# Kernel tuning notes

Measured on AMD Instinct MI355X. Metric: run time of the kernel, lower is better.

The kernel has to match this reference:

```python
import jax, jax.numpy as jnp
import numpy as np

M = 16                      # multiplicity of each irrep block
INV3 = 1.0 / np.sqrt(3.0)   # w3j(1,1,0) component-normalized
INV2 = 1.0 / np.sqrt(2.0)   # w3j(1,1,1) component-normalized
A0 = 1.0 / np.sqrt(2.0 * M) # fan-in norm for 0e outputs (2 paths x mul 16)
A1 = 1.0 / np.sqrt(3.0 * M) # fan-in norm for 1o outputs (3 paths x mul 16)


def setup_inputs() -> dict:
    E, N, ED, HID = 100000, 10000, 32, 128
    WNUM = 2 * M * (2 * M) + 3 * M * M  # 1792 per-edge TP weights
    ks = jax.random.split(jax.random.key(0), 10)
    return {
        "dst": jax.random.randint(ks[0], (E,), 0, N),
        "x_src": jax.random.normal(ks[1], (E, 4 * M), jnp.float32),   # 16x0e+16x1o
        "x_dst": jax.random.normal(ks[2], (N, 4 * M), jnp.float32),
        "sh": jax.random.normal(ks[3], (E, 4), jnp.float32),          # 1x0e+1x1o
        "edge_attr": jax.random.normal(ks[4], (E, ED), jnp.float32),
        "We1": jax.random.normal(ks[5], (ED, HID), jnp.float32) / np.sqrt(ED),
        "be1": jnp.zeros((HID,), jnp.float32),
        "We2": jax.random.normal(ks[6], (HID, WNUM), jnp.float32) / np.sqrt(HID),
        "be2": jnp.zeros((WNUM,), jnp.float32),
        "Wr0": jax.random.normal(ks[7], (M, 2 * M), jnp.float32),     # 16x0e -> 32x0e
        "Wr1": jax.random.normal(ks[8], (M, M), jnp.float32),         # 16x1o -> 16x1o
    }


def _forward(dst, x_src, x_dst, sh, edge_attr, We1, be1, We2, be2, Wr0, Wr1):
    E = x_src.shape[0]
    N = x_dst.shape[0]
    o0 = 2 * M  # 32x0e tp output (scalars + gates)

    # edge MLP -> per-edge tensor-product weights [E, 1792]
    w = jax.nn.relu(edge_attr @ We1 + be1) @ We2 + be2
    i = 0
    w_ss = w[:, i:i + M * o0].reshape(E, M, o0); i += M * o0   # 0e x 0e -> 0e
    w_vv0 = w[:, i:i + M * o0].reshape(E, M, o0); i += M * o0  # 1o x 1o -> 0e
    w_sv = w[:, i:i + M * M].reshape(E, M, M); i += M * M      # 0e x 1o -> 1o
    w_vs = w[:, i:i + M * M].reshape(E, M, M); i += M * M      # 1o x 0e -> 1o
    w_vv1 = w[:, i:i + M * M].reshape(E, M, M)                 # 1o x 1o -> 1o

    s1 = x_src[:, :M]                       # [E, 16]
    v1 = x_src[:, M:].reshape(E, M, 3)      # [E, 16, 3]
    s2 = sh[:, 0]                           # [E]
    v2 = sh[:, 1:4]                         # [E, 3]

    # fully-connected tensor product with per-edge weights
    out0 = A0 * (jnp.einsum('em,emo->eo', s1 * s2[:, None], w_ss)
                 + INV3 * jnp.einsum('emc,ec,emo->eo', v1, v2, w_vv0))  # [E, 32]
    cross = jnp.cross(v1, v2[:, None, :])   # [E, 16, 3]
    out1 = A1 * (jnp.einsum('em,ec,emo->eoc', s1, v2, w_sv)
                 + jnp.einsum('emc,e,emo->eoc', v1, s2, w_vs)
                 + INV2 * jnp.einsum('emc,emo->eoc', cross, w_vv1))     # [E, 16, 3]
    msg = jnp.concatenate([out0, out1.reshape(E, -1)], axis=1)          # [E, 80]

    # scatter-mean over destination nodes
    ssum = jax.ops.segment_sum(msg, dst, num_segments=N)
    cnt = jax.ops.segment_sum(jnp.ones((E,), msg.dtype), dst, num_segments=N)
    msg = ssum / jnp.maximum(cnt, 1.0)[:, None]                          # [N, 80]

    # residual equivariant linear on x_dst
    sd = x_dst[:, :M]
    vd = x_dst[:, M:].reshape(N, M, 3)
    res0 = (sd @ Wr0) / np.sqrt(M)                                       # [N, 32]
    res1 = jnp.einsum('nmc,mo->noc', vd, Wr1) / np.sqrt(M)               # [N, 16, 3]
    msg = msg + jnp.concatenate([res0, res1.reshape(N, -1)], axis=1)

    # gate nonlinearity: relu(scalars), sigmoid(gates) * gated vectors
    scalars = jax.nn.relu(msg[:, :M])
    gates = jax.nn.sigmoid(msg[:, M:2 * M])
    gated = msg[:, 2 * M:].reshape(N, M, 3) * gates[:, :, None]
    return jnp.concatenate([scalars, gated.reshape(N, -1)], axis=1)      # [N, 64]


def reference(dst, x_src, x_dst, sh, edge_attr, We1, be1, We2, be2, Wr0, Wr1):
    return _forward(dst, x_src, x_dst, sh, edge_attr, We1, be1, We2, be2, Wr0, Wr1)
```

## Files before the change

### kernel.cpp

```cpp
#include <hip/hip_runtime.h>
#include <math.h>

#define WNUM 1792
#define HID 128

#define INV3C 0.5773502691896258f
#define INV2C 0.7071067811865476f
#define A0C   0.17677669529663687f
#define A1C   0.14433756729740643f
#define MAXDEG 64

typedef short bf8 __attribute__((ext_vector_type(8)));
typedef _Float16 f16x8 __attribute__((ext_vector_type(8)));
typedef _Float16 f16x4 __attribute__((ext_vector_type(4)));
typedef float f32x4 __attribute__((ext_vector_type(4)));

__device__ inline unsigned short f2bf(float f) {
  union { float f; unsigned u; } v; v.f = f;
  unsigned r = v.u + 0x7FFFu + ((v.u >> 16) & 1u);
  return (unsigned short)(r >> 16);
}
__device__ inline float bf2f(unsigned short h) {
  union { unsigned u; float f; } v; v.u = ((unsigned)h) << 16;
  return v.f;
}
__device__ inline float wscale(int t) {
  if (t < 32) return A0C;
  if (t < 64) return A0C * INV3C;
  if (t < 96) return A1C;
  return A1C * INV2C;
}

__global__ __launch_bounds__(256) void prep_kernel(
    const float* __restrict__ We1, const float* __restrict__ We2,
    const float* __restrict__ be2,
    unsigned short* __restrict__ we1x, _Float16* __restrict__ we2h,
    float* __restrict__ be2p, int* __restrict__ cntp, int N)
{
  int i = blockIdx.x * 256 + threadIdx.x;
  if (i < 28672) {
    int t = i >> 8, c = (i >> 6) & 3, lane = i & 63;
    int quad = lane >> 4, l15 = lane & 15;
    int col = t * 16 + l15;
    float sc = wscale(t);
    f16x8 v;
    #pragma unroll
    for (int j = 0; j < 8; ++j) {
      int k = c * 32 + quad * 8 + j;
      v[j] = (_Float16)(We2[(size_t)k * WNUM + col] * sc);
    }
    *(f16x8*)(we2h + (size_t)t * 2048 + c * 512 + lane * 8) = v;
  } else if (i < 29184) {
    int q = i - 28672;
    int c1 = q >> 6, lane = q & 63;
    int quad = lane >> 4, l15 = lane & 15;
    int col = c1 * 16 + l15;
    bf8 hh, ll;
    #pragma unroll
    for (int j = 0; j < 8; ++j) {
      int k = quad * 8 + j;
      float v = We1[k * HID + col];
      unsigned short hi = f2bf(v);
      hh[j] = (short)hi;
      ll[j] = (short)f2bf(v - bf2f(hi));
    }
    *(bf8*)(we1x + c1 * 1024 + lane * 8) = hh;
    *(bf8*)(we1x + c1 * 1024 + 512 + lane * 8) = ll;
  } else if (i < 30976) {
    int q = i - 29184;
    int t = q >> 4, l16 = q & 15;
    be2p[(t >> 1) * 32 + l16 * 2 + (t & 1)] = be2[q] * wscale(t);
  } else if (i < 30976 + N) {
    cntp[i - 30976] = 0;
  }
}

__device__ inline void chains2(const f16x8* a0, const f16x8* a1,
    f16x8 b0, f16x8 b1, f16x8 b2, f16x8 b3,
    f16x8 b4, f16x8 b5, f16x8 b6, f16x8 b7,
    float2 bias, f32x4* wa, f32x4* wb)
{
  f32x4 ca0 = {bias.x, bias.x, bias.x, bias.x};
  f32x4 cb0 = {bias.y, bias.y, bias.y, bias.y};
  f32x4 ca1 = ca0, cb1 = cb0;
  ca0 = __builtin_amdgcn_mfma_f32_16x16x32_f16(a0[0], b0, ca0, 0, 0, 0);
  cb0 = __builtin_amdgcn_mfma_f32_16x16x32_f16(a0[0], b4, cb0, 0, 0, 0);
  ca1 = __builtin_amdgcn_mfma_f32_16x16x32_f16(a1[0], b0, ca1, 0, 0, 0);
  cb1 = __builtin_amdgcn_mfma_f32_16x16x32_f16(a1[0], b4, cb1, 0, 0, 0);
  ca0 = __builtin_amdgcn_mfma_f32_16x16x32_f16(a0[1], b1, ca0, 0, 0, 0);
  cb0 = __builtin_amdgcn_mfma_f32_16x16x32_f16(a0[1], b5, cb0, 0, 0, 0);
  ca1 = __builtin_amdgcn_mfma_f32_16x16x32_f16(a1[1], b1, ca1, 0, 0, 0);
  cb1 = __builtin_amdgcn_mfma_f32_16x16x32_f16(a1[1], b5, cb1, 0, 0, 0);
  ca0 = __builtin_amdgcn_mfma_f32_16x16x32_f16(a0[2], b2, ca0, 0, 0, 0);
  cb0 = __builtin_amdgcn_mfma_f32_16x16x32_f16(a0[2], b6, cb0, 0, 0, 0);
  ca1 = __builtin_amdgcn_mfma_f32_16x16x32_f16(a1[2], b2, ca1, 0, 0, 0);
  cb1 = __builtin_amdgcn_mfma_f32_16x16x32_f16(a1[2], b6, cb1, 0, 0, 0);
  ca0 = __builtin_amdgcn_mfma_f32_16x16x32_f16(a0[3], b3, ca0, 0, 0, 0);
  cb0 = __builtin_amdgcn_mfma_f32_16x16x32_f16(a0[3], b7, cb0, 0, 0, 0);
  ca1 = __builtin_amdgcn_mfma_f32_16x16x32_f16(a1[3], b3, ca1, 0, 0, 0);
  cb1 = __builtin_amdgcn_mfma_f32_16x16x32_f16(a1[3], b7, cb1, 0, 0, 0);
  wa[0] = ca0; wb[0] = cb0; wa[1] = ca1; wb[1] = cb1;
}

__device__ inline void pair_mm(const _Float16* bL, const float* bp, int p,
                               const f16x8 (&af)[2][4], f32x4* wa, f32x4* wb)
{
  f16x8 b0 = *(const f16x8*)(bL);
  f16x8 b1 = *(const f16x8*)(bL + 512);
  f16x8 b2 = *(const f16x8*)(bL + 1024);
  f16x8 b3 = *(const f16x8*)(bL + 1536);
  f16x8 b4 = *(const f16x8*)(bL + 2048);
  f16x8 b5 = *(const f16x8*)(bL + 2560);
  f16x8 b6 = *(const f16x8*)(bL + 3072);
  f16x8 b7 = *(const f16x8*)(bL + 3584);
  float2 bias2 = *(const float2*)(bp + p * 32);
  chains2(af[0], af[1], b0, b1, b2, b3, b4, b5, b6, b7, bias2, wa, wb);
}

template <bool MSG>
__global__ __launch_bounds__(256, 2) void edge_kernel(
    const float* __restrict__ ea, const float* __restrict__ xsrc,
    const float* __restrict__ sh, const int* __restrict__ dst,
    const float* __restrict__ be1,
    const unsigned short* __restrict__ we1x, const _Float16* __restrict__ we2h,
    const float* __restrict__ be2p,
    float* __restrict__ outp, int* __restrict__ eidx, int* __restrict__ cntp, int E)
{
  const int lane = threadIdx.x & 63;
  const int w    = threadIdx.x >> 6;
  const int quad = lane >> 4;
  const int l16  = lane & 15;
  const int eb   = (blockIdx.x * 4 + w) * 32;

  __shared__ union SMem {
    _Float16 h[4][32][136];
    _Float16 B[4][4096];
  } uS;
  __shared__ _Float16 fss_s[4][16][32];
  __shared__ _Float16 fvv_s[4][16][32];
  __shared__ _Float16 s1h_s[4][16][32];
  __shared__ _Float16 v1h_s[4][16][3][32];
  __shared__ float4 vq_s[4][32];

  #define STAGE_PAIR(p) { \
    const _Float16* gsrc_ = we2h + (size_t)(p) * 4096; \
    _Float16* ldst_ = &uS.B[(p) & 3][0]; \
    __builtin_amdgcn_global_load_lds( \
      (const __attribute__((address_space(1))) void*)(gsrc_ + (w * 2) * 512 + lane * 8), \
      (__attribute__((address_space(3))) void*)(ldst_ + (w * 2) * 512), 16, 0, 0); \
    __builtin_amdgcn_global_load_lds( \
      (const __attribute__((address_space(1))) void*)(gsrc_ + (w * 2 + 1) * 512 + lane * 8), \
      (__attribute__((address_space(3))) void*)(ldst_ + (w * 2 + 1) * 512), 16, 0, 0); \
  }

  if (lane < 32) {
    int ge = eb + lane;
    if (ge < E) {
      int node = dst[ge];
      int pos = atomicAdd(cntp + node, 1);
      if (MSG) { if (pos < MAXDEG) eidx[node * MAXDEG + pos] = ge; }
    }
  }

  {
    int e2 = lane >> 1, mg = lane & 1;
    int ge = eb + e2;
    if (ge < E) {
      const float* xp = xsrc + (size_t)ge * 64;
      float4 sq0 = *(const float4*)(xp + mg * 8);
      float4 sq1 = *(const float4*)(xp + mg * 8 + 4);
      float s1a[8] = {sq0.x,sq0.y,sq0.z,sq0.w,sq1.x,sq1.y,sq1.z,sq1.w};
      const float* vp = xp + 16 + mg * 24;
      float la[24];
      #pragma unroll
      for (int qv = 0; qv < 6; ++qv) {
        float4 t = *(const float4*)(vp + qv * 4);
        la[qv*4+0] = t.x; la[qv*4+1] = t.y; la[qv*4+2] = t.z; la[qv*4+3] = t.w;
      }
      float4 shq = *(const float4*)(sh + (size_t)ge * 4);
      float s2 = shq.x, v2x = shq.y, v2y = shq.z, v2z = shq.w;
      #pragma unroll
      for (int mi = 0; mi < 8; ++mi) {
        int m = mg * 8 + mi;
        float v1x = la[mi*3], v1y = la[mi*3+1], v1z = la[mi*3+2];
        fss_s[w][m][e2] = (_Float16)(s1a[mi] * s2);
        fvv_s[w][m][e2] = (_Float16)(v1x*v2x + v1y*v2y + v1z*v2z);
        s1h_s[w][m][e2] = (_Float16)s1a[mi];
        v1h_s[w][m][0][e2] = (_Float16)v1x;
        v1h_s[w][m][1][e2] = (_Float16)v1y;
        v1h_s[w][m][2][e2] = (_Float16)v1z;
      }
      if (mg == 0) vq_s[w][e2] = make_float4(v2x, v2y, v2z, s2);
    } else {
      #pragma unroll
      for (int mi = 0; mi < 8; ++mi) {
        int m = mg * 8 + mi;
        fss_s[w][m][e2] = (_Float16)0.f;
        fvv_s[w][m][e2] = (_Float16)0.f;
        s1h_s[w][m][e2] = (_Float16)0.f;
        v1h_s[w][m][0][e2] = (_Float16)0.f;
        v1h_s[w][m][1][e2] = (_Float16)0.f;
        v1h_s[w][m][2][e2] = (_Float16)0.f;
      }
      if (mg == 0) vq_s[w][e2] = make_float4(0,0,0,0);
    }
  }

  {
    bf8 ah[2], al[2];
    #pragma unroll
    for (int g = 0; g < 2; ++g) {
      int gea = eb + g * 16 + l16; if (gea > E - 1) gea = E - 1;
      const float* ep = ea + (size_t)gea * 32 + quad * 8;
      float4 p0 = *(const float4*)ep;
      float4 p1 = *(const float4*)(ep + 4);
      float pv[8] = {p0.x,p0.y,p0.z,p0.w,p1.x,p1.y,p1.z,p1.w};
      #pragma unroll
      for (int j = 0; j < 8; ++j) {
        unsigned short hi = f2bf(pv[j]);
        ah[g][j] = (short)hi;
        al[g][j] = (short)f2bf(pv[j] - bf2f(hi));
      }
    }
    const unsigned short* wb1 = we1x + lane * 8;
    #pragma unroll 2
    for (int c = 0; c < 8; ++c) {
      bf8 bh = *(const bf8*)(wb1 + c * 1024);
      bf8 bl = *(const bf8*)(wb1 + c * 1024 + 512);
      float bias = be1[c * 16 + l16];
      #pragma unroll
      for (int g = 0; g < 2; ++g) {
        f32x4 hc = {bias, bias, bias, bias};
        hc = __builtin_amdgcn_mfma_f32_16x16x32_bf16(al[g], bh, hc, 0, 0, 0);
        hc = __builtin_amdgcn_mfma_f32_16x16x32_bf16(ah[g], bl, hc, 0, 0, 0);
        hc = __builtin_amdgcn_mfma_f32_16x16x32_bf16(ah[g], bh, hc, 0, 0, 0);
        #pragma unroll
        for (int r = 0; r < 4; ++r)
          uS.h[w][g * 16 + quad * 4 + r][c * 16 + l16] = (_Float16)fmaxf(hc[r], 0.f);
      }
    }
  }
  __syncthreads();

  f16x8 af[2][4];
  #pragma unroll
  for (int g = 0; g < 2; ++g)
    #pragma unroll
    for (int ch = 0; ch < 4; ++ch)
      af[g][ch] = *(const f16x8*)&uS.h[w][g * 16 + l16][ch * 32 + quad * 8];
  __syncthreads();

  STAGE_PAIR(0)
  STAGE_PAIR(1)
  __syncthreads();

  const float* bp = be2p + l16 * 2;
  float m0a[2][4] = {{0,0,0,0},{0,0,0,0}}, m0b[2][4] = {{0,0,0,0},{0,0,0,0}};

  #pragma unroll 1
  for (int i = 0; i < 16; i += 2) {
    STAGE_PAIR(i + 2)
    STAGE_PAIR(i + 3)
    f32x4 wa[2], wb[2];
    pair_mm(&uS.B[i & 3][lane * 8], bp, i, af, wa, wb);
    #pragma unroll
    for (int g = 0; g < 2; ++g) {
      f16x4 fv = *(const f16x4*)&fss_s[w][i][g * 16 + quad * 4];
      #pragma unroll
      for (int r = 0; r < 4; ++r) {
        float f = (float)fv[r];
        m0a[g][r] = fmaf(wa[g][r], f, m0a[g][r]);
        m0b[g][r] = fmaf(wb[g][r], f, m0b[g][r]);
      }
    }
    pair_mm(&uS.B[(i + 1) & 3][lane * 8], bp, i + 1, af, wa, wb);
    #pragma unroll
    for (int g = 0; g < 2; ++g) {
      f16x4 fv = *(const f16x4*)&fss_s[w][i + 1][g * 16 + quad * 4];
      #pragma unroll
      for (int r = 0; r < 4; ++r) {
        float f = (float)fv[r];
        m0a[g][r] = fmaf(wa[g][r], f, m0a[g][r]);
        m0b[g][r] = fmaf(wb[g][r], f, m0b[g][r]);
      }
    }
    __syncthreads();
  }

  #pragma unroll 1
  for (int i = 0; i < 16; i += 2) {
    int pg = 16 + i;
    STAGE_PAIR(pg + 2)
    STAGE_PAIR(pg + 3)
    f32x4 wa[2], wb[2];
    pair_mm(&uS.B[pg & 3][lane * 8], bp, pg, af, wa, wb);
    #pragma unroll
    for (int g = 0; g < 2; ++g) {
      f16x4 fv = *(const f16x4*)&fvv_s[w][i][g * 16 + quad * 4];
      #pragma unroll
      for (int r = 0; r < 4; ++r) {
        float f = (float)fv[r];
        m0a[g][r] = fmaf(wa[g][r], f, m0a[g][r]);
        m0b[g][r] = fmaf(wb[g][r], f, m0b[g][r]);
      }
    }
    pair_mm(&uS.B[(pg + 1) & 3][lane * 8], bp, pg + 1, af, wa, wb);
    #pragma unroll
    for (int g = 0; g < 2; ++g) {
      f16x4 fv = *(const f16x4*)&fvv_s[w][i + 1][g * 16 + quad * 4];
      #pragma unroll
      for (int r = 0; r < 4; ++r) {
        float f = (float)fv[r];
        m0a[g][r] = fmaf(wa[g][r], f, m0a[g][r]);
        m0b[g][r] = fmaf(wb[g][r], f, m0b[g][r]);
      }
    }
    __syncthreads();
  }

  #pragma unroll
  for (int g = 0; g < 2; ++g)
    #pragma unroll
    for (int r = 0; r < 4; ++r) {
      int ge = eb + g * 16 + quad * 4 + r;
      if (ge < E) {
        if (MSG) {
          float* mp = outp + (size_t)ge * 80;
          mp[l16]      = m0a[g][r];
          mp[16 + l16] = m0b[g][r];
        } else {
          float* ap = outp + (size_t)dst[ge] * 80;
          atomicAdd(ap + l16,      m0a[g][r]);
          atomicAdd(ap + 16 + l16, m0b[g][r]);
        }
      }
    }

  float sg[2][4] = {{0,0,0,0},{0,0,0,0}};
  #pragma unroll 1
  for (int i = 0; i < 8; i += 2) {
    int pg = 32 + i;
    STAGE_PAIR(pg + 2)
    STAGE_PAIR(pg + 3)
    f32x4 wa[2], wb[2];
    pair_mm(&uS.B[pg & 3][lane * 8], bp, pg, af, wa, wb);
    #pragma unroll
    for (int g = 0; g < 2; ++g) {
      f16x4 sA = *(const f16x4*)&s1h_s[w][2*i][g * 16 + quad * 4];
      f16x4 sB = *(const f16x4*)&s1h_s[w][2*i + 1][g * 16 + quad * 4];
      #pragma unroll
      for (int r = 0; r < 4; ++r)
        sg[g][r] = fmaf(wb[g][r], (float)sB[r], fmaf(wa[g][r], (float)sA[r], sg[g][r]));
    }
    pair_mm(&uS.B[(pg + 1) & 3][lane * 8], bp, pg + 1, af, wa, wb);
    #pragma unroll
    for (int g = 0; g < 2; ++g) {
      f16x4 sA = *(const f16x4*)&s1h_s[w][2*i + 2][g * 16 + quad * 4];
      f16x4 sB = *(const f16x4*)&s1h_s[w][2*i + 3][g * 16 + quad * 4];
      #pragma unroll
      for (int r = 0; r < 4; ++r)
        sg[g][r] = fmaf(wb[g][r], (float)sB[r], fmaf(wa[g][r], (float)sA[r], sg[g][r]));
    }
    __syncthreads();
  }
  float4 vq[2][4];
  #pragma unroll
  for (int g = 0; g < 2; ++g)
    #pragma unroll
    for (int r = 0; r < 4; ++r) vq[g][r] = vq_s[w][g * 16 + quad * 4 + r];

  float m1x[2][4], m1y[2][4], m1z[2][4];
  #pragma unroll
  for (int g = 0; g < 2; ++g)
    #pragma unroll
    for (int r = 0; r < 4; ++r) {
      m1x[g][r] = sg[g][r] * vq[g][r].x;
      m1y[g][r] = sg[g][r] * vq[g][r].y;
      m1z[g][r] = sg[g][r] * vq[g][r].z;
    }

  #pragma unroll
  for (int sec = 0; sec < 2; ++sec) {
    float ux[2][4] = {{0,0,0,0},{0,0,0,0}}, uy[2][4] = {{0,0,0,0},{0,0,0,0}},
          uz[2][4] = {{0,0,0,0},{0,0,0,0}};
    int base = 40 + sec * 8;
    #pragma unroll 1
    for (int i = 0; i < 8; i += 2) {
      int pg = base + i;
      if (pg + 2 < 56) STAGE_PAIR(pg + 2)
      if (pg + 3 < 56) STAGE_PAIR(pg + 3)
      f32x4 wa[2], wb[2];
      pair_mm(&uS.B[pg & 3][lane * 8], bp, pg, af, wa, wb);
      #pragma unroll
      for (int g = 0; g < 2; ++g) {
        f16x4 xA = *(const f16x4*)&v1h_s[w][2*i][0][g*16 + quad*4];
        f16x4 xB = *(const f16x4*)&v1h_s[w][2*i+1][0][g*16 + quad*4];
        f16x4 yA = *(const f16x4*)&v1h_s[w][2*i][1][g*16 + quad*4];
        f16x4 yB = *(const f16x4*)&v1h_s[w][2*i+1][1][g*16 + quad*4];
        f16x4 zA = *(const f16x4*)&v1h_s[w][2*i][2][g*16 + quad*4];
        f16x4 zB = *(const f16x4*)&v1h_s[w][2*i+1][2][g*16 + quad*4];
        #pragma unroll
        for (int r = 0; r < 4; ++r) {
          ux[g][r] = fmaf(wb[g][r], (float)xB[r], fmaf(wa[g][r], (float)xA[r], ux[g][r]));
          uy[g][r] = fmaf(wb[g][r], (float)yB[r], fmaf(wa[g][r], (float)yA[r], uy[g][r]));
          uz[g][r] = fmaf(wb[g][r], (float)zB[r], fmaf(wa[g][r], (float)zA[r], uz[g][r]));
        }
      }
      pair_mm(&uS.B[(pg + 1) & 3][lane * 8], bp, pg + 1, af, wa, wb);
      #pragma unroll
      for (int g = 0; g < 2; ++g) {
        f16x4 xA = *(const f16x4*)&v1h_s[w][2*i+2][0][g*16 + quad*4];
        f16x4 xB = *(const f16x4*)&v1h_s[w][2*i+3][0][g*16 + quad*4];
        f16x4 yA = *(const f16x4*)&v1h_s[w][2*i+2][1][g*16 + quad*4];
        f16x4 yB = *(const f16x4*)&v1h_s[w][2*i+3][1][g*16 + quad*4];
        f16x4 zA = *(const f16x4*)&v1h_s[w][2*i+2][2][g*16 + quad*4];
        f16x4 zB = *(const f16x4*)&v1h_s[w][2*i+3][2][g*16 + quad*4];
        #pragma unroll
        for (int r = 0; r < 4; ++r) {
          ux[g][r] = fmaf(wb[g][r], (float)xB[r], fmaf(wa[g][r], (float)xA[r], ux[g][r]));
          uy[g][r] = fmaf(wb[g][r], (float)yB[r], fmaf(wa[g][r], (float)yA[r], uy[g][r]));
          uz[g][r] = fmaf(wb[g][r], (float)zB[r], fmaf(wa[g][r], (float)zA[r], uz[g][r]));
        }
      }
      __syncthreads();
    }
    if (sec == 0) {
      #pragma unroll
      for (int g = 0; g < 2; ++g)
        #pragma unroll
        for (int r = 0; r < 4; ++r) {
          m1x[g][r] = fmaf(vq[g][r].w, ux[g][r], m1x[g][r]);
          m1y[g][r] = fmaf(vq[g][r].w, uy[g][r], m1y[g][r]);
          m1z[g][r] = fmaf(vq[g][r].w, uz[g][r], m1z[g][r]);
        }
    } else {
      #pragma unroll
      for (int g = 0; g < 2; ++g)
        #pragma unroll
        for (int r = 0; r < 4; ++r) {
          m1x[g][r] = fmaf(uy[g][r], vq[g][r].z, m1x[g][r]);
          m1x[g][r] = fmaf(-uz[g][r], vq[g][r].y, m1x[g][r]);
          m1y[g][r] = fmaf(uz[g][r], vq[g][r].x, m1y[g][r]);
          m1y[g][r] = fmaf(-ux[g][r], vq[g][r].z, m1y[g][r]);
          m1z[g][r] = fmaf(ux[g][r], vq[g][r].y, m1z[g][r]);
          m1z[g][r] = fmaf(-uy[g][r], vq[g][r].x, m1z[g][r]);
        }
    }
  }

  #pragma unroll
  for (int g = 0; g < 2; ++g)
    #pragma unroll
    for (int r = 0; r < 4; ++r) {
      int ge = eb + g * 16 + quad * 4 + r;
      if (ge < E) {
        if (MSG) {
          float* mp = outp + (size_t)ge * 80;
          mp[32 + l16*3 + 0] = m1x[g][r];
          mp[32 + l16*3 + 1] = m1y[g][r];
          mp[32 + l16*3 + 2] = m1z[g][r];
        } else {
          float* ap = outp + (size_t)dst[ge] * 80;
          atomicAdd(ap + 32 + l16*3 + 0, m1x[g][r]);
          atomicAdd(ap + 32 + l16*3 + 1, m1y[g][r]);
          atomicAdd(ap + 32 + l16*3 + 2, m1z[g][r]);
        }
      }
    }
  #undef STAGE_PAIR
}

__global__ __launch_bounds__(128) void node_gather_kernel(
    const float* __restrict__ msg, const int* __restrict__ eidx,
    const int* __restrict__ cntp,
    const float* __restrict__ xdst, const float* __restrict__ Wr0,
    const float* __restrict__ Wr1, float* __restrict__ out, int N)
{
  int n = blockIdx.x;
  if (n >= N) return;
  int j = threadIdx.x;
  int c0 = cntp[n];
  int deg = c0 < MAXDEG ? c0 : MAXDEG;
  float inv = 1.0f / fmaxf((float)c0, 1.0f);
  __shared__ float s_sum[80];
  if (j < 80) {
    float s = 0.f;
    const int* ep = eidx + (size_t)n * MAXDEG;
    int i = 0;
    for (; i + 1 < deg; i += 2) {
      int e0 = ep[i], e1 = ep[i + 1];
      s += msg[(size_t)e0 * 80 + j] + msg[(size_t)e1 * 80 + j];
    }
    if (i < deg) s += msg[(size_t)ep[i] * 80 + j];
    s_sum[j] = s * inv;
  }
  __syncthreads();
  if (j >= 64) return;
  const float* xd = xdst + (size_t)n * 64;
  float* op = out + (size_t)n * 64;
  if (j < 16) {
    float s = 0.f;
    #pragma unroll
    for (int m = 0; m < 16; ++m) s = fmaf(xd[m], Wr0[m * 32 + j], s);
    op[j] = fmaxf(s_sum[j] + 0.25f * s, 0.f);
  } else {
    int jj = j - 16;
    int o = (jj * 86) >> 8;
    int c = jj - o * 3;
    float tg = 0.f, v = 0.f;
    #pragma unroll
    for (int m = 0; m < 16; ++m) {
      tg = fmaf(xd[m], Wr0[m * 32 + 16 + o], tg);
      v  = fmaf(xd[16 + m * 3 + c], Wr1[m * 16 + o], v);
    }
    float g = 1.0f / (1.0f + expf(-(s_sum[16 + o] + 0.25f * tg)));
    op[16 + jj] = (s_sum[32 + jj] + 0.25f * v) * g;
  }
}

__global__ __launch_bounds__(256) void node_kernel(
    const float* __restrict__ accn, const int* __restrict__ cntp,
    const float* __restrict__ xdst, const float* __restrict__ Wr0,
    const float* __restrict__ Wr1, float* __restrict__ out, int N)
{
  int idx = blockIdx.x * 256 + threadIdx.x;
  int n = idx >> 6, j = idx & 63;
  if (n >= N) return;
  float inv = 1.0f / fmaxf((float)cntp[n], 1.0f);
  const float* ap = accn + (size_t)n * 80;
  const float* xd = xdst + (size_t)n * 64;
  float* op = out + (size_t)n * 64;
  if (j < 16) {
    float s = 0.f;
    #pragma unroll
    for (int m = 0; m < 16; ++m) s = fmaf(xd[m], Wr0[m * 32 + j], s);
    op[j] = fmaxf(ap[j] * inv + 0.25f * s, 0.f);
  } else {
    int jj = j - 16;
    int o = (jj * 86) >> 8;
    int c = jj - o * 3;
    float tg = 0.f, v = 0.f;
    #pragma unroll
    for (int m = 0; m < 16; ++m) {
      tg = fmaf(xd[m], Wr0[m * 32 + 16 + o], tg);
      v  = fmaf(xd[16 + m * 3 + c], Wr1[m * 16 + o], v);
    }
    float g = 1.0f / (1.0f + expf(-(ap[16 + o] * inv + 0.25f * tg)));
    op[16 + jj] = (ap[32 + jj] * inv + 0.25f * v) * g;
  }
}

extern "C" void kernel_launch(void* const* d_in, const int* in_sizes, int n_in,
                              void* d_out, int out_size, void* d_ws, size_t ws_size,
                              hipStream_t stream)
{
  const int*   dst  = (const int*)d_in[0];
  const float* xsrc = (const float*)d_in[1];
  const float* xdst = (const float*)d_in[2];
  const float* sh   = (const float*)d_in[3];
  const float* ea   = (const float*)d_in[4];
  const float* We1  = (const float*)d_in[5];
  const float* be1  = (const float*)d_in[6];
  const float* We2  = (const float*)d_in[7];
  const float* be2  = (const float*)d_in[8];
  const float* Wr0  = (const float*)d_in[9];
  const float* Wr1  = (const float*)d_in[10];
  const int E = in_sizes[0];
  const int N = in_sizes[2] / 64;

  char* ws = (char*)d_ws;
  _Float16* we2h = (_Float16*)ws;
  unsigned short* we1x = (unsigned short*)(ws + 458752);
  float* be2p = (float*)(ws + 475136);
  int*   cntp = (int*)(ws + 482560);
  size_t off = 482560 + (size_t)N * 4;
  off = (off + 15) & ~(size_t)15;

  size_t need_msg = off + (size_t)N * MAXDEG * 4 + (size_t)E * 80 * 4;
  bool use_msg = (ws_size >= need_msg);

  prep_kernel<<<(30976 + N + 255) / 256, 256, 0, stream>>>(We1, We2, be2,
      we1x, we2h, be2p, cntp, N);

  if (use_msg) {
    int* eidx = (int*)(ws + off);
    float* msg = (float*)(ws + off + (size_t)N * MAXDEG * 4);
    edge_kernel<true><<<(E + 127) / 128, 256, 0, stream>>>(ea, xsrc, sh, dst, be1,
        we1x, we2h, be2p, msg, eidx, cntp, E);
    node_gather_kernel<<<N, 128, 0, stream>>>(msg, eidx, cntp, xdst, Wr0, Wr1,
        (float*)d_out, N);
  } else {
    float* accn = (float*)(ws + off);
    hipMemsetAsync(accn, 0, (size_t)N * 320, stream);
    edge_kernel<false><<<(E + 127) / 128, 256, 0, stream>>>(ea, xsrc, sh, dst, be1,
        we1x, we2h, be2p, accn, (int*)nullptr, cntp, E);
    node_kernel<<<((size_t)N * 64 + 255) / 256, 256, 0, stream>>>(accn, cntp,
        xdst, Wr0, Wr1, (float*)d_out, N);
  }
}
```

Before: 199.5 us.

## Merge weight-generation phases into one loop with deeper staging and partial waitcnt barriers

Replaces the four separate loops over weight pairs (two steps per iteration, full __syncthreads) with a single 56-step loop. The loop stages pairs three ahead into the 4-slot ring buffer and syncs with explicit s_waitcnt on vmcnt plus s_barrier, so the newest global loads can stay in flight across the barrier. The aim is to keep more weight-staging loads outstanding and cut barrier drain stalls. In exchange the loop body carries branches on the phase index and holds all accumulators live at once, which raises register pressure, and the hand-coded waitcnt immediates must match the real number of loads issued per stage.

```diff
diff --git a/kernel.cpp b/kernel.cpp
--- a/kernel.cpp
+++ b/kernel.cpp
@@ -248,157 +248,76 @@
     #pragma unroll
     for (int ch = 0; ch < 4; ++ch)
       af[g][ch] = *(const f16x8*)&uS.h[w][g * 16 + l16][ch * 32 + quad * 8];
-  __syncthreads();
-
-  STAGE_PAIR(0)
-  STAGE_PAIR(1)
-  __syncthreads();
-
-  const float* bp = be2p + l16 * 2;
-  float m0a[2][4] = {{0,0,0,0},{0,0,0,0}}, m0b[2][4] = {{0,0,0,0},{0,0,0,0}};
-
-  #pragma unroll 1
-  for (int i = 0; i < 16; i += 2) {
-    STAGE_PAIR(i + 2)
-    STAGE_PAIR(i + 3)
-    f32x4 wa[2], wb[2];
-    pair_mm(&uS.B[i & 3][lane * 8], bp, i, af, wa, wb);
-    #pragma unroll
-    for (int g = 0; g < 2; ++g) {
-      f16x4 fv = *(const f16x4*)&fss_s[w][i][g * 16 + quad * 4];
-      #pragma unroll
-      for (int r = 0; r < 4; ++r) {
-        float f = (float)fv[r];
-        m0a[g][r] = fmaf(wa[g][r], f, m0a[g][r]);
-        m0b[g][r] = fmaf(wb[g][r], f, m0b[g][r]);
-      }
-    }
-    pair_mm(&uS.B[(i + 1) & 3][lane * 8], bp, i + 1, af, wa, wb);
-    #pragma unroll
-    for (int g = 0; g < 2; ++g) {
-      f16x4 fv = *(const f16x4*)&fss_s[w][i + 1][g * 16 + quad * 4];
-      #pragma unroll
-      for (int r = 0; r < 4; ++r) {
-        float f = (float)fv[r];
-        m0a[g][r] = fmaf(wa[g][r], f, m0a[g][r]);
-        m0b[g][r] = fmaf(wb[g][r], f, m0b[g][r]);
-      }
-    }
-    __syncthreads();
-  }
-
-  #pragma unroll 1
-  for (int i = 0; i < 16; i += 2) {
-    int pg = 16 + i;
-    STAGE_PAIR(pg + 2)
-    STAGE_PAIR(pg + 3)
-    f32x4 wa[2], wb[2];
-    pair_mm(&uS.B[pg & 3][lane * 8], bp, pg, af, wa, wb);
-    #pragma unroll
-    for (int g = 0; g < 2; ++g) {
-      f16x4 fv = *(const f16x4*)&fvv_s[w][i][g * 16 + quad * 4];
-      #pragma unroll
-      for (int r = 0; r < 4; ++r) {
-        float f = (float)fv[r];
-        m0a[g][r] = fmaf(wa[g][r], f, m0a[g][r]);
-        m0b[g][r] = fmaf(wb[g][r], f, m0b[g][r]);
-      }
-    }
-    pair_mm(&uS.B[(pg + 1) & 3][lane * 8], bp, pg + 1, af, wa, wb);
-    #pragma unroll
-    for (int g = 0; g < 2; ++g) {
-      f16x4 fv = *(const f16x4*)&fvv_s[w][i + 1][g * 16 + quad * 4];
-      #pragma unroll
-      for (int r = 0; r < 4; ++r) {
-        float f = (float)fv[r];
-        m0a[g][r] = fmaf(wa[g][r], f, m0a[g][r]);
-        m0b[g][r] = fmaf(wb[g][r], f, m0b[g][r]);
-      }
-    }
-    __syncthreads();
-  }
-
-  #pragma unroll
-  for (int g = 0; g < 2; ++g)
-    #pragma unroll
-    for (int r = 0; r < 4; ++r) {
-      int ge = eb + g * 16 + quad * 4 + r;
-      if (ge < E) {
-        if (MSG) {
-          float* mp = outp + (size_t)ge * 80;
-          mp[l16]      = m0a[g][r];
-          mp[16 + l16] = m0b[g][r];
-        } else {
-          float* ap = outp + (size_t)dst[ge] * 80;
-          atomicAdd(ap + l16,      m0a[g][r]);
-          atomicAdd(ap + 16 + l16, m0b[g][r]);
-        }
-      }
-    }
-
-  float sg[2][4] = {{0,0,0,0},{0,0,0,0}};
-  #pragma unroll 1
-  for (int i = 0; i < 8; i += 2) {
-    int pg = 32 + i;
-    STAGE_PAIR(pg + 2)
-    STAGE_PAIR(pg + 3)
-    f32x4 wa[2], wb[2];
-    pair_mm(&uS.B[pg & 3][lane * 8], bp, pg, af, wa, wb);
-    #pragma unroll
-    for (int g = 0; g < 2; ++g) {
-      f16x4 sA = *(const f16x4*)&s1h_s[w][2*i][g * 16 + quad * 4];
-      f16x4 sB = *(const f16x4*)&s1h_s[w][2*i + 1][g * 16 + quad * 4];
-      #pragma unroll
-      for (int r = 0; r < 4; ++r)
-        sg[g][r] = fmaf(wb[g][r], (float)sB[r], fmaf(wa[g][r], (float)sA[r], sg[g][r]));
-    }
-    pair_mm(&uS.B[(pg + 1) & 3][lane * 8], bp, pg + 1, af, wa, wb);
-    #pragma unroll
-    for (int g = 0; g < 2; ++g) {
-      f16x4 sA = *(const f16x4*)&s1h_s[w][2*i + 2][g * 16 + quad * 4];
-      f16x4 sB = *(const f16x4*)&s1h_s[w][2*i + 3][g * 16 + quad * 4];
-      #pragma unroll
-      for (int r = 0; r < 4; ++r)
-        sg[g][r] = fmaf(wb[g][r], (float)sB[r], fmaf(wa[g][r], (float)sA[r], sg[g][r]));
-    }
-    __syncthreads();
-  }
+
   float4 vq[2][4];
   #pragma unroll
   for (int g = 0; g < 2; ++g)
     #pragma unroll
     for (int r = 0; r < 4; ++r) vq[g][r] = vq_s[w][g * 16 + quad * 4 + r];
-
+  __syncthreads();
+
+  STAGE_PAIR(0)
+  STAGE_PAIR(1)
+  STAGE_PAIR(2)
+  __builtin_amdgcn_s_waitcnt(0xF74);
+  __builtin_amdgcn_s_barrier();
+
+  const float* bp = be2p + l16 * 2;
+  float m0a[2][4] = {{0,0,0,0},{0,0,0,0}}, m0b[2][4] = {{0,0,0,0},{0,0,0,0}};
+  float sg[2][4]  = {{0,0,0,0},{0,0,0,0}};
+  float ux[2][4]  = {{0,0,0,0},{0,0,0,0}}, uy[2][4] = {{0,0,0,0},{0,0,0,0}},
+        uz[2][4]  = {{0,0,0,0},{0,0,0,0}};
   float m1x[2][4], m1y[2][4], m1z[2][4];
-  #pragma unroll
-  for (int g = 0; g < 2; ++g)
-    #pragma unroll
-    for (int r = 0; r < 4; ++r) {
-      m1x[g][r] = sg[g][r] * vq[g][r].x;
-      m1y[g][r] = sg[g][r] * vq[g][r].y;
-      m1z[g][r] = sg[g][r] * vq[g][r].z;
-    }
-
-  #pragma unroll
-  for (int sec = 0; sec < 2; ++sec) {
-    float ux[2][4] = {{0,0,0,0},{0,0,0,0}}, uy[2][4] = {{0,0,0,0},{0,0,0,0}},
-          uz[2][4] = {{0,0,0,0},{0,0,0,0}};
-    int base = 40 + sec * 8;
-    #pragma unroll 1
-    for (int i = 0; i < 8; i += 2) {
-      int pg = base + i;
-      if (pg + 2 < 56) STAGE_PAIR(pg + 2)
-      if (pg + 3 < 56) STAGE_PAIR(pg + 3)
-      f32x4 wa[2], wb[2];
-      pair_mm(&uS.B[pg & 3][lane * 8], bp, pg, af, wa, wb);
+
+  #pragma unroll 1
+  for (int p = 0; p < 56; ++p) {
+    if (p + 3 < 56) STAGE_PAIR(p + 3)
+
+    f32x4 wa[2], wb[2];
+    pair_mm(&uS.B[p & 3][lane * 8], bp, p, af, wa, wb);
+
+    if (p < 16) {
       #pragma unroll
       for (int g = 0; g < 2; ++g) {
-        f16x4 xA = *(const f16x4*)&v1h_s[w][2*i][0][g*16 + quad*4];
-        f16x4 xB = *(const f16x4*)&v1h_s[w][2*i+1][0][g*16 + quad*4];
-        f16x4 yA = *(const f16x4*)&v1h_s[w][2*i][1][g*16 + quad*4];
-        f16x4 yB = *(const f16x4*)&v1h_s[w][2*i+1][1][g*16 + quad*4];
-        f16x4 zA = *(const f16x4*)&v1h_s[w][2*i][2][g*16 + quad*4];
-        f16x4 zB = *(const f16x4*)&v1h_s[w][2*i+1][2][g*16 + quad*4];
+        f16x4 fv = *(const f16x4*)&fss_s[w][p][g * 16 + quad * 4];
+        #pragma unroll
+        for (int r = 0; r < 4; ++r) {
+          float f = (float)fv[r];
+          m0a[g][r] = fmaf(wa[g][r], f, m0a[g][r]);
+          m0b[g][r] = fmaf(wb[g][r], f, m0b[g][r]);
+        }
+      }
+    } else if (p < 32) {
+      #pragma unroll
+      for (int g = 0; g < 2; ++g) {
+        f16x4 fv = *(const f16x4*)&fvv_s[w][p - 16][g * 16 + quad * 4];
+        #pragma unroll
+        for (int r = 0; r < 4; ++r) {
+          float f = (float)fv[r];
+          m0a[g][r] = fmaf(wa[g][r], f, m0a[g][r]);
+          m0b[g][r] = fmaf(wb[g][r], f, m0b[g][r]);
+        }
+      }
+    } else if (p < 40) {
+      int j = 2 * (p - 32);
+      #pragma unroll
+      for (int g = 0; g < 2; ++g) {
+        f16x4 sA = *(const f16x4*)&s1h_s[w][j][g * 16 + quad * 4];
+        f16x4 sB = *(const f16x4*)&s1h_s[w][j + 1][g * 16 + quad * 4];
+        #pragma unroll
+        for (int r = 0; r < 4; ++r)
+          sg[g][r] = fmaf(wb[g][r], (float)sB[r], fmaf(wa[g][r], (float)sA[r], sg[g][r]));
+      }
+    } else {
+      int j = 2 * (p - (p < 48 ? 40 : 48));
+      #pragma unroll
+      for (int g = 0; g < 2; ++g) {
+        f16x4 xA = *(const f16x4*)&v1h_s[w][j][0][g*16 + quad*4];
+        f16x4 xB = *(const f16x4*)&v1h_s[w][j+1][0][g*16 + quad*4];
+        f16x4 yA = *(const f16x4*)&v1h_s[w][j][1][g*16 + quad*4];
+        f16x4 yB = *(const f16x4*)&v1h_s[w][j+1][1][g*16 + quad*4];
+        f16x4 zA = *(const f16x4*)&v1h_s[w][j][2][g*16 + quad*4];
+        f16x4 zB = *(const f16x4*)&v1h_s[w][j+1][2][g*16 + quad*4];
         #pragma unroll
         for (int r = 0; r < 4; ++r) {
           ux[g][r] = fmaf(wb[g][r], (float)xB[r], fmaf(wa[g][r], (float)xA[r], ux[g][r]));
@@ -406,25 +325,40 @@
           uz[g][r] = fmaf(wb[g][r], (float)zB[r], fmaf(wa[g][r], (float)zA[r], uz[g][r]));
         }
       }
-      pair_mm(&uS.B[(pg + 1) & 3][lane * 8], bp, pg + 1, af, wa, wb);
-      #pragma unroll
-      for (int g = 0; g < 2; ++g) {
-        f16x4 xA = *(const f16x4*)&v1h_s[w][2*i+2][0][g*16 + quad*4];
-        f16x4 xB = *(const f16x4*)&v1h_s[w][2*i+3][0][g*16 + quad*4];
-        f16x4 yA = *(const f16x4*)&v1h_s[w][2*i+2][1][g*16 + quad*4];
-        f16x4 yB = *(const f16x4*)&v1h_s[w][2*i+3][1][g*16 + quad*4];
-        f16x4 zA = *(const f16x4*)&v1h_s[w][2*i+2][2][g*16 + quad*4];
-        f16x4 zB = *(const f16x4*)&v1h_s[w][2*i+3][2][g*16 + quad*4];
+    }
+
+    if (p < 53) __builtin_amdgcn_s_waitcnt(0xF72);
+    else        __builtin_amdgcn_s_waitcnt(0xF70);
+    __builtin_amdgcn_s_barrier();
+
+    if (p == 31) {
+      #pragma unroll
+      for (int g = 0; g < 2; ++g)
         #pragma unroll
         for (int r = 0; r < 4; ++r) {
-          ux[g][r] = fmaf(wb[g][r], (float)xB[r], fmaf(wa[g][r], (float)xA[r], ux[g][r]));
-          uy[g][r] = fmaf(wb[g][r], (float)yB[r], fmaf(wa[g][r], (float)yA[r], uy[g][r]));
-          uz[g][r] = fmaf(wb[g][r], (float)zB[r], fmaf(wa[g][r], (float)zA[r], uz[g][r]));
-        }
-      }
-      __syncthreads();
-    }
-    if (sec == 0) {
+          int ge = eb + g * 16 + quad * 4 + r;
+          if (ge < E) {
+            if (MSG) {
+              float* mp = outp + (size_t)ge * 80;
+              mp[l16]      = m0a[g][r];
+              mp[16 + l16] = m0b[g][r];
+            } else {
+              float* ap = outp + (size_t)dst[ge] * 80;
+              atomicAdd(ap + l16,      m0a[g][r]);
+              atomicAdd(ap + 16 + l16, m0b[g][r]);
+            }
+          }
+        }
+    } else if (p == 39) {
+      #pragma unroll
+      for (int g = 0; g < 2; ++g)
+        #pragma unroll
+        for (int r = 0; r < 4; ++r) {
+          m1x[g][r] = sg[g][r] * vq[g][r].x;
+          m1y[g][r] = sg[g][r] * vq[g][r].y;
+          m1z[g][r] = sg[g][r] * vq[g][r].z;
+        }
+    } else if (p == 47) {
       #pragma unroll
       for (int g = 0; g < 2; ++g)
         #pragma unroll
@@ -432,21 +366,22 @@
           m1x[g][r] = fmaf(vq[g][r].w, ux[g][r], m1x[g][r]);
           m1y[g][r] = fmaf(vq[g][r].w, uy[g][r], m1y[g][r]);
           m1z[g][r] = fmaf(vq[g][r].w, uz[g][r], m1z[g][r]);
-        }
-    } else {
-      #pragma unroll
-      for (int g = 0; g < 2; ++g)
-        #pragma unroll
-        for (int r = 0; r < 4; ++r) {
-          m1x[g][r] = fmaf(uy[g][r], vq[g][r].z, m1x[g][r]);
-          m1x[g][r] = fmaf(-uz[g][r], vq[g][r].y, m1x[g][r]);
-          m1y[g][r] = fmaf(uz[g][r], vq[g][r].x, m1y[g][r]);
-          m1y[g][r] = fmaf(-ux[g][r], vq[g][r].z, m1y[g][r]);
-          m1z[g][r] = fmaf(ux[g][r], vq[g][r].y, m1z[g][r]);
-          m1z[g][r] = fmaf(-uy[g][r], vq[g][r].x, m1z[g][r]);
-        }
-    }
-  }
+          ux[g][r] = 0.f; uy[g][r] = 0.f; uz[g][r] = 0.f;
+        }
+    }
+  }
+
+  #pragma unroll
+  for (int g = 0; g < 2; ++g)
+    #pragma unroll
+    for (int r = 0; r < 4; ++r) {
+      m1x[g][r] = fmaf(uy[g][r], vq[g][r].z, m1x[g][r]);
+      m1x[g][r] = fmaf(-uz[g][r], vq[g][r].y, m1x[g][r]);
+      m1y[g][r] = fmaf(uz[g][r], vq[g][r].x, m1y[g][r]);
+      m1y[g][r] = fmaf(-ux[g][r], vq[g][r].z, m1y[g][r]);
+      m1z[g][r] = fmaf(ux[g][r], vq[g][r].y, m1z[g][r]);
+      m1z[g][r] = fmaf(-uy[g][r], vq[g][r].x, m1z[g][r]);
+    }
 
   #pragma unroll
   for (int g = 0; g < 2; ++g)
```

After: 271.4 us. 36.0% more time.
